# Optimization experiments

Measured on AMD Instinct MI355X. Metric: run time of the kernel, lower is better.

Reference implementation:

```python
import jax, jax.numpy as jnp
import numpy as np

N_NODES = 100000
N_EDGES = 1600000
DIM = 64
N_GRAPHS = 1000


def setup_inputs() -> dict:
    key = jax.random.key(0)
    ks = jax.random.split(key, 6)
    s = 1.0 / np.sqrt(DIM)
    x = jax.random.normal(ks[0], (N_NODES, DIM), dtype=jnp.float32)
    edge_index = jax.random.randint(ks[1], (2, N_EDGES), 0, N_NODES, dtype=jnp.int64)
    batch = jnp.sort(jax.random.randint(ks[2], (N_NODES,), 0, N_GRAPHS, dtype=jnp.int64))
    W1 = jax.random.normal(ks[3], (DIM, DIM), dtype=jnp.float32) * s
    b1 = jnp.zeros((DIM,), jnp.float32)
    W2 = jax.random.normal(ks[4], (DIM, DIM), dtype=jnp.float32) * s
    b2 = jnp.zeros((DIM,), jnp.float32)
    return {"x": x, "W1": W1, "b1": b1, "W2": W2, "b2": b2,
            "edge_index": edge_index, "batch": batch}


def reference(x, W1, b1, W2, b2, edge_index, batch):
    n = x.shape[0]
    loop = jnp.arange(n, dtype=edge_index.dtype)
    src = jnp.concatenate([edge_index[0], loop])  # [E+N] with self-loops
    dst = jnp.concatenate([edge_index[1], loop])
    # symmetric GCN normalization: deg^{-1/2}[src] * deg^{-1/2}[dst]
    deg = jax.ops.segment_sum(jnp.ones(src.shape[0], x.dtype), dst, num_segments=n)
    dinv = jax.lax.rsqrt(jnp.maximum(deg, 1.0))  # deg >= 1 due to self-loops
    norm = (dinv[src] * dinv[dst])[:, None]      # [E+N, 1]

    def gcn(h, W, b):
        h = h @ W                                  # transform first (smaller dim path)
        msg = h[src] * norm                        # gather + normalize
        return jax.ops.segment_sum(msg, dst, num_segments=n) + b

    h = jax.nn.relu(gcn(x, W1, b1))
    # dropout: eval mode -> identity
    h = jax.nn.relu(gcn(h, W2, b2))

    counts = jax.ops.segment_sum(jnp.ones((n,), x.dtype), batch, num_segments=N_GRAPHS)
    pooled = jax.ops.segment_sum(h, batch, num_segments=N_GRAPHS)
    return pooled / jnp.maximum(counts, 1.0)[:, None]
```

## Files before the change

kernel.cpp:

```cpp
#include <hip/hip_runtime.h>
#include <hip/hip_fp16.h>

#define DIM 64
#define BIN_SHIFT 7
#define BINSZ 128
#define MAXBINS 1024
#define PB 128

typedef __attribute__((ext_vector_type(2))) float floatx2;
typedef __attribute__((ext_vector_type(4))) float f32x4;
typedef __attribute__((ext_vector_type(8))) _Float16 f16x8;
typedef __attribute__((ext_vector_type(4))) _Float16 f16x4;


__global__ __launch_bounds__(256) void k_zero(int* __restrict__ bintot,
                                              float* __restrict__ out,
                                              int NB, int GD) {
    int i = blockIdx.x * 256 + threadIdx.x;
    if (i < NB) bintot[i] = 0;
    for (int j = i; j < GD; j += gridDim.x * 256) out[j] = 0.f;
}


__global__ __launch_bounds__(256) void k_hist2(const int* __restrict__ dst,
                                               int* __restrict__ bintot, int E, int NB) {
    __shared__ int h[MAXBINS];
    for (int i = threadIdx.x; i < NB; i += 256) h[i] = 0;
    __syncthreads();
    int per = (E + PB - 1) / PB;
    int e0 = blockIdx.x * per;
    int e1 = e0 + per; if (e1 > E) e1 = E;
    for (int e = e0 + (int)threadIdx.x; e < e1; e += 256)
        atomicAdd(&h[dst[e] >> BIN_SHIFT], 1);
    __syncthreads();
    for (int i = threadIdx.x; i < NB; i += 256)
        if (h[i]) atomicAdd(&bintot[i], h[i]);
}


__global__ __launch_bounds__(256) void k_scan782(const int* __restrict__ bintot,
                                                 int* __restrict__ binoff,
                                                 int* __restrict__ bincur, int NB, int E) {
    __shared__ int ws[4];
    int tid = threadIdx.x;
    int j0 = tid * 4;
    int v[4]; int sum = 0;
#pragma unroll
    for (int t = 0; t < 4; ++t) {
        int j = j0 + t;
        int x = (j < NB) ? bintot[j] : 0;
        v[t] = sum; sum += x;
    }
    int lane = tid & 63, wv = tid >> 6;
    int x = sum;
#pragma unroll
    for (int d = 1; d < 64; d <<= 1) {
        int t = __shfl_up(x, d);
        if (lane >= d) x += t;
    }
    if (lane == 63) ws[wv] = x;
    __syncthreads();
    int prefix = 0;
    for (int w = 0; w < wv; ++w) prefix += ws[w];
    int ex = prefix + x - sum;
#pragma unroll
    for (int t = 0; t < 4; ++t) {
        int j = j0 + t;
        if (j < NB) { binoff[j] = ex + v[t]; bincur[j] = ex + v[t]; }
    }
    if (tid == 255) binoff[NB] = prefix + x;
}


__global__ __launch_bounds__(256) void k_bucket2(const int* __restrict__ src,
                                                 const int* __restrict__ dst,
                                                 int* __restrict__ bincur,
                                                 int* __restrict__ bkt, int E, int NB) {
    __shared__ int cnt_[MAXBINS], base_[MAXBINS];
    int tid = threadIdx.x;
    for (int i = tid; i < NB; i += 256) cnt_[i] = 0;
    __syncthreads();
    int per = (E + PB - 1) / PB;
    int e0 = blockIdx.x * per;
    int e1 = e0 + per; if (e1 > E) e1 = E;
    for (int e = e0 + tid; e < e1; e += 256)
        atomicAdd(&cnt_[dst[e] >> BIN_SHIFT], 1);
    __syncthreads();
    for (int i = tid; i < NB; i += 256) {
        int c = cnt_[i];
        base_[i] = c ? atomicAdd(&bincur[i], c) : 0;
        cnt_[i] = 0;
    }
    __syncthreads();
    for (int e = e0 + tid; e < e1; e += 256) {
        int d = dst[e];
        int b = d >> BIN_SHIFT;
        int pos = base_[b] + atomicAdd(&cnt_[b], 1);
        bkt[pos] = src[e] | ((d & (BINSZ - 1)) << 24);
    }
}


__global__ __launch_bounds__(256) void k_binsort(const int* __restrict__ bkt,
                                                 const int* __restrict__ binoff,
                                                 int* __restrict__ csr,
                                                 int* __restrict__ off,
                                                 float* __restrict__ dinv,
                                                 const int* __restrict__ batch,
                                                 int* __restrict__ goff,
                                                 int N, int G, int E, int NB) {
    __shared__ int cnt[BINSZ], bas[BINSZ], cur[BINSZ];
    __shared__ int wsum[4];
    int tid = threadIdx.x;
    int b = blockIdx.x;
    int s0 = binoff[b];
    int s1 = binoff[b + 1];
    if (tid < BINSZ) { cnt[tid] = 0; cur[tid] = 0; }
    __syncthreads();
    for (int i = s0 + tid; i < s1; i += 256)
        atomicAdd(&cnt[(bkt[i] >> 24) & (BINSZ - 1)], 1);
    __syncthreads();
    int my = (tid < BINSZ) ? cnt[tid] : 0;
    int lane = tid & 63, wv = tid >> 6;
    int x = my;
#pragma unroll
    for (int d = 1; d < 64; d <<= 1) {
        int t = __shfl_up(x, d);
        if (lane >= d) x += t;
    }
    if (lane == 63) wsum[wv] = x;
    __syncthreads();
    int prefix = 0;
    for (int w = 0; w < wv; ++w) prefix += wsum[w];
    int ex = x + prefix - my;
    if (tid < BINSZ) {
        bas[tid] = ex;
        int v = (b << BIN_SHIFT) + tid;
        if (v < N) {
            off[v] = s0 + ex;
            dinv[v] = rsqrtf((float)(my + 1));
            if (v == N - 1) off[N] = E;
            int bb = batch[v];
            int prev = (v == 0) ? -1 : batch[v - 1];
            for (int g = prev + 1; g <= bb; ++g) goff[g] = v;
            if (v == N - 1)
                for (int g = bb + 1; g <= G; ++g) goff[g] = N;
        }
    }
    __syncthreads();
    for (int i = s0 + tid; i < s1; i += 256) {
        int p = bkt[i];
        int lo = (p >> 24) & (BINSZ - 1);
        int li = atomicAdd(&cur[lo], 1);
        csr[s0 + bas[lo] + li] = p & 0xFFFFFF;
    }
}


__global__ __launch_bounds__(256) void k_gemm(const float* __restrict__ X,
                                              const float* __restrict__ W,
                                              const float* __restrict__ dinv,
                                              unsigned int* __restrict__ Y8, int N) {
    __shared__ float Os[16 * 68];
    int tid = threadIdx.x;
    int lane = tid & 63, w = tid >> 6;
    int m = lane & 15, g = lane >> 4;
    int row0 = blockIdx.x * 16;
    int row = row0 + m;

    f16x8 B0, B1;
    {
        int n = (w << 4) + m;
        const float* wp = W + (g << 3) * 64 + n;
#pragma unroll
        for (int j = 0; j < 8; ++j) B0[j] = (_Float16)wp[j * 64];
        wp += 32 * 64;
#pragma unroll
        for (int j = 0; j < 8; ++j) B1[j] = (_Float16)wp[j * 64];
    }
    f16x8 A0, A1;
    {
        float4 u0 = make_float4(0.f, 0.f, 0.f, 0.f), u1 = u0, u2 = u0, u3 = u0;
        if (row < N) {
            const float* xp = X + (size_t)row * DIM + (g << 3);
            u0 = *(const float4*)(xp);
            u1 = *(const float4*)(xp + 4);
            u2 = *(const float4*)(xp + 32);
            u3 = *(const float4*)(xp + 36);
        }
        A0[0] = (_Float16)u0.x; A0[1] = (_Float16)u0.y; A0[2] = (_Float16)u0.z; A0[3] = (_Float16)u0.w;
        A0[4] = (_Float16)u1.x; A0[5] = (_Float16)u1.y; A0[6] = (_Float16)u1.z; A0[7] = (_Float16)u1.w;
        A1[0] = (_Float16)u2.x; A1[1] = (_Float16)u2.y; A1[2] = (_Float16)u2.z; A1[3] = (_Float16)u2.w;
        A1[4] = (_Float16)u3.x; A1[5] = (_Float16)u3.y; A1[6] = (_Float16)u3.z; A1[7] = (_Float16)u3.w;
    }
    f32x4 acc = {0.f, 0.f, 0.f, 0.f};
    acc = __builtin_amdgcn_mfma_f32_16x16x32_f16(A0, B0, acc, 0, 0, 0);
    acc = __builtin_amdgcn_mfma_f32_16x16x32_f16(A1, B1, acc, 0, 0, 0);
#pragma unroll
    for (int j = 0; j < 4; ++j)
        Os[((g << 2) + j) * 68 + (w << 4) + m] = acc[j];
    __syncthreads();

    int r = tid >> 4, c = tid & 15;
    int orow = row0 + r;
    if (orow < N) {
        float4 o = *(const float4*)(Os + r * 68 + (c << 2));
        float s = dinv[orow];
        int p = 0;
        p = __builtin_amdgcn_cvt_pk_fp8_f32(o.x * s, o.y * s, p, false);
        p = __builtin_amdgcn_cvt_pk_fp8_f32(o.z * s, o.w * s, p, true);
        Y8[(size_t)orow * 16 + c] = (unsigned int)p;
    } else if (orow == N) {
        Y8[(size_t)orow * 16 + c] = 0u;
    }
}


__device__ __forceinline__ float4 gather_rows(const unsigned int* __restrict__ hs8,
                                              const int* __restrict__ csr,
                                              int k0, int k1, int v, int l, int gw4,
                                              int N) {
    float4 a0, a1, a2, a3;
    {
        unsigned int u = hs8[(unsigned)((v << 4) | l)];
        floatx2 f0 = __builtin_amdgcn_cvt_pk_f32_fp8((int)u, false);
        floatx2 f1 = __builtin_amdgcn_cvt_pk_f32_fp8((int)u, true);
        a0 = make_float4(f0.x, f0.y, f1.x, f1.y);
        a1 = make_float4(0.f, 0.f, 0.f, 0.f);
        a2 = make_float4(0.f, 0.f, 0.f, 0.f);
        a3 = make_float4(0.f, 0.f, 0.f, 0.f);
    }
    for (int kb = k0; kb < k1; kb += 16) {
        int rem = k1 - kb;
        int idx = (l < rem) ? csr[kb + l] : N;
        unsigned uu[16];
#pragma unroll
        for (int t = 0; t < 16; ++t) {
            int s = __shfl(idx, gw4 + t);
            uu[t] = hs8[(unsigned)((s << 4) | l)];
        }
#pragma unroll
        for (int t = 0; t < 16; t += 4) {
            floatx2 q0 = __builtin_amdgcn_cvt_pk_f32_fp8((int)uu[t + 0], false);
            floatx2 q1 = __builtin_amdgcn_cvt_pk_f32_fp8((int)uu[t + 0], true);
            floatx2 q2 = __builtin_amdgcn_cvt_pk_f32_fp8((int)uu[t + 1], false);
            floatx2 q3 = __builtin_amdgcn_cvt_pk_f32_fp8((int)uu[t + 1], true);
            floatx2 q4 = __builtin_amdgcn_cvt_pk_f32_fp8((int)uu[t + 2], false);
            floatx2 q5 = __builtin_amdgcn_cvt_pk_f32_fp8((int)uu[t + 2], true);
            floatx2 q6 = __builtin_amdgcn_cvt_pk_f32_fp8((int)uu[t + 3], false);
            floatx2 q7 = __builtin_amdgcn_cvt_pk_f32_fp8((int)uu[t + 3], true);
            a0.x += q0.x; a0.y += q0.y; a0.z += q1.x; a0.w += q1.y;
            a1.x += q2.x; a1.y += q2.y; a1.z += q3.x; a1.w += q3.y;
            a2.x += q4.x; a2.y += q4.y; a2.z += q5.x; a2.w += q5.y;
            a3.x += q6.x; a3.y += q6.y; a3.z += q7.x; a3.w += q7.y;
        }
    }
    return make_float4(a0.x + a1.x + a2.x + a3.x,
                       a0.y + a1.y + a2.y + a3.y,
                       a0.z + a1.z + a2.z + a3.z,
                       a0.w + a1.w + a2.w + a3.w);
}


__global__ __launch_bounds__(256) void k_gather_gemm(const unsigned int* __restrict__ hs8,
                                                     const int* __restrict__ csr,
                                                     const int* __restrict__ off,
                                                     const float* __restrict__ dinv,
                                                     const float* __restrict__ bias,
                                                     const float* __restrict__ W,
                                                     unsigned int* __restrict__ hs_out,
                                                     int N) {
    __shared__ _Float16 Xs[16 * 72];
    __shared__ float Os[16 * 68];
    int tid = threadIdx.x;
    int r = tid >> 4, l = tid & 15;
    int lane = tid & 63, w = tid >> 6;
    int m = lane & 15, g = lane >> 4;
    int gw4 = (r & 3) << 4;
    int v = blockIdx.x * 16 + r;

    f16x8 B0, B1;
    {
        int n = (w << 4) + m;
        const float* wp = W + (g << 3) * 64 + n;
#pragma unroll
        for (int j = 0; j < 8; ++j) B0[j] = (_Float16)wp[j * 64];
        wp += 32 * 64;
#pragma unroll
        for (int j = 0; j < 8; ++j) B1[j] = (_Float16)wp[j * 64];
    }
    if (blockIdx.x == 0 && tid < 16)
        hs_out[(size_t)N * 16 + tid] = 0u;

    float dv = 0.f;
    float4 h = make_float4(0.f, 0.f, 0.f, 0.f);
    if (v < N) {
        dv = dinv[v];
        float4 bv = ((const float4*)bias)[l];
        float4 acc = gather_rows(hs8, csr, off[v], off[v + 1], v, l, gw4, N);
        h.x = fmaxf(acc.x * dv + bv.x, 0.f);
        h.y = fmaxf(acc.y * dv + bv.y, 0.f);
        h.z = fmaxf(acc.z * dv + bv.z, 0.f);
        h.w = fmaxf(acc.w * dv + bv.w, 0.f);
    }
    {
        f16x4 hv;
        hv[0] = (_Float16)h.x; hv[1] = (_Float16)h.y;
        hv[2] = (_Float16)h.z; hv[3] = (_Float16)h.w;
        *(f16x4*)(Xs + r * 72 + (l << 2)) = hv;
    }
    __syncthreads();

    f16x8 A0 = *(const f16x8*)(Xs + m * 72 + (g << 3));
    f16x8 A1 = *(const f16x8*)(Xs + m * 72 + 32 + (g << 3));
    f32x4 acc2 = {0.f, 0.f, 0.f, 0.f};
    acc2 = __builtin_amdgcn_mfma_f32_16x16x32_f16(A0, B0, acc2, 0, 0, 0);
    acc2 = __builtin_amdgcn_mfma_f32_16x16x32_f16(A1, B1, acc2, 0, 0, 0);
#pragma unroll
    for (int j = 0; j < 4; ++j)
        Os[((g << 2) + j) * 68 + (w << 4) + m] = acc2[j];
    __syncthreads();

    if (v < N) {
        float4 o = *(const float4*)(Os + r * 68 + (l << 2));
        int p = 0;
        p = __builtin_amdgcn_cvt_pk_fp8_f32(o.x * dv, o.y * dv, p, false);
        p = __builtin_amdgcn_cvt_pk_fp8_f32(o.z * dv, o.w * dv, p, true);
        hs_out[(size_t)v * 16 + l] = (unsigned int)p;
    }
}


__global__ __launch_bounds__(256) void k_gather_pool(const unsigned int* __restrict__ hs8,
                                                     const int* __restrict__ csr,
                                                     const int* __restrict__ off,
                                                     const float* __restrict__ dinv,
                                                     const float* __restrict__ bias,
                                                     const int* __restrict__ batch,
                                                     const int* __restrict__ goff,
                                                     float* __restrict__ out, int N) {
    __shared__ float vals[16][68];
    __shared__ int gid[16];
    int tid = threadIdx.x;
    int r = tid >> 4, l = tid & 15;
    int gw4 = (r & 3) << 4;
    int v = blockIdx.x * 16 + r;

    float4 val = make_float4(0.f, 0.f, 0.f, 0.f);
    int g = -1;
    if (v < N) {
        g = batch[v];
        float dv = dinv[v];
        float4 bv = ((const float4*)bias)[l];
        float4 acc = gather_rows(hs8, csr, off[v], off[v + 1], v, l, gw4, N);
        float inv = 1.0f / (float)(goff[g + 1] - goff[g]);
        val.x = fmaxf(acc.x * dv + bv.x, 0.f) * inv;
        val.y = fmaxf(acc.y * dv + bv.y, 0.f) * inv;
        val.z = fmaxf(acc.z * dv + bv.z, 0.f) * inv;
        val.w = fmaxf(acc.w * dv + bv.w, 0.f) * inv;
    }
    *(float4*)(&vals[r][l << 2]) = val;
    if (l == 0) gid[r] = g;
    __syncthreads();

    if (v < N) {
        bool leader = (r == 0) || (gid[r - 1] != g);
        if (leader) {
            float4 sacc = val;
            for (int rr = r + 1; rr < 16 && gid[rr] == g; ++rr) {
                float4 t = *(const float4*)(&vals[rr][l << 2]);
                sacc.x += t.x; sacc.y += t.y; sacc.z += t.z; sacc.w += t.w;
            }
            float* op = out + (size_t)g * DIM + (l << 2);
            atomicAdd(op + 0, sacc.x);
            atomicAdd(op + 1, sacc.y);
            atomicAdd(op + 2, sacc.z);
            atomicAdd(op + 3, sacc.w);
        }
    }
}


static inline int cdiv(int a, int b) { return (a + b - 1) / b; }

extern "C" void kernel_launch(void* const* d_in, const int* in_sizes, int n_in,
                              void* d_out, int out_size, void* d_ws, size_t ws_size,
                              hipStream_t stream) {
    const float* x   = (const float*)d_in[0];
    const float* W1  = (const float*)d_in[1];
    const float* b1  = (const float*)d_in[2];
    const float* W2  = (const float*)d_in[3];
    const float* b2  = (const float*)d_in[4];
    const int*   ei  = (const int*)d_in[5];
    const int*   bat = (const int*)d_in[6];

    const int N = in_sizes[0] / DIM;
    const int E = in_sizes[5] / 2;
    const int G = out_size / DIM;
    const int NB = cdiv(N, BINSZ);
    const int* src = ei;
    const int* dst = ei + E;
    float* out = (float*)d_out;

    __half* hs1    = (__half*)d_ws;
    __half* hs2    = hs1 + (size_t)(N + 1) * DIM;
    float*  dinv   = (float*)(hs2 + (size_t)(N + 1) * DIM);
    int*    off    = (int*)(dinv + N);
    int*    goff   = off + (N + 1);
    int*    bintot = goff + (G + 1);
    int*    binoff = bintot + MAXBINS;
    int*    bincur = binoff + (MAXBINS + 1);
    int*    csr    = bincur + MAXBINS;
    int*    bkt    = (int*)hs1;

    k_zero<<<256, 256, 0, stream>>>(bintot, out, NB, G * DIM);
    k_hist2<<<PB, 256, 0, stream>>>(dst, bintot, E, NB);
    k_scan782<<<1, 256, 0, stream>>>(bintot, binoff, bincur, NB, E);
    k_bucket2<<<PB, 256, 0, stream>>>(src, dst, bincur, bkt, E, NB);
    k_binsort<<<NB, 256, 0, stream>>>(bkt, binoff, csr, off, dinv, bat, goff, N, G, E, NB);

    k_gemm<<<cdiv(N + 1, 16), 256, 0, stream>>>(x, W1, dinv, (unsigned int*)hs1, N);

    k_gather_gemm<<<cdiv(N, 16), 256, 0, stream>>>((const unsigned int*)hs1, csr, off,
                                                   dinv, b1, W2, (unsigned int*)hs2, N);

    k_gather_pool<<<cdiv(N, 16), 256, 0, stream>>>((const unsigned int*)hs2, csr, off,
                                                   dinv, b2, bat, goff, out, N);
}
```

Baseline: 221.7 us.

## Replace two-level binned CSR build with global atomic counting sort

Replaces the histogram, bucket and per-bin LDS sort pipeline with a simpler counting sort. A per-node degree pass uses global atomics, a two-kernel block scan builds offsets (also computing dinv and graph offsets), and a scatter places each source into CSR through a global atomicAdd on the per-node cursor. This drops the intermediate bucket array and the bin-sort kernel. In exchange it trades LDS atomics and localized writes for millions of global atomics and random scattered CSR writes, and neighbour order within a row becomes nondeterministic.

New measurement: 349.3 us. +57.6%, slower.

```diff
diff --git a/kernel.cpp b/kernel.cpp
--- a/kernel.cpp
+++ b/kernel.cpp
@@ -2,10 +2,6 @@
 #include <hip/hip_fp16.h>
 
 #define DIM 64
-#define BIN_SHIFT 7
-#define BINSZ 128
-#define MAXBINS 1024
-#define PB 128
 
 typedef __attribute__((ext_vector_type(2))) float floatx2;
 typedef __attribute__((ext_vector_type(4))) float f32x4;
@@ -13,42 +9,36 @@
 typedef __attribute__((ext_vector_type(4))) _Float16 f16x4;
 
 
-__global__ __launch_bounds__(256) void k_zero(int* __restrict__ bintot,
+__global__ __launch_bounds__(256) void k_zero(int* __restrict__ deg,
                                               float* __restrict__ out,
-                                              int NB, int GD) {
+                                              int N, int GD) {
     int i = blockIdx.x * 256 + threadIdx.x;
-    if (i < NB) bintot[i] = 0;
-    for (int j = i; j < GD; j += gridDim.x * 256) out[j] = 0.f;
-}
-
-
-__global__ __launch_bounds__(256) void k_hist2(const int* __restrict__ dst,
-                                               int* __restrict__ bintot, int E, int NB) {
-    __shared__ int h[MAXBINS];
-    for (int i = threadIdx.x; i < NB; i += 256) h[i] = 0;
-    __syncthreads();
-    int per = (E + PB - 1) / PB;
-    int e0 = blockIdx.x * per;
-    int e1 = e0 + per; if (e1 > E) e1 = E;
-    for (int e = e0 + (int)threadIdx.x; e < e1; e += 256)
-        atomicAdd(&h[dst[e] >> BIN_SHIFT], 1);
-    __syncthreads();
-    for (int i = threadIdx.x; i < NB; i += 256)
-        if (h[i]) atomicAdd(&bintot[i], h[i]);
-}
-
-
-__global__ __launch_bounds__(256) void k_scan782(const int* __restrict__ bintot,
-                                                 int* __restrict__ binoff,
-                                                 int* __restrict__ bincur, int NB, int E) {
-    __shared__ int ws[4];
+    int stride = gridDim.x * 256;
+    for (int j = i; j < N; j += stride) deg[j] = 0;
+    for (int j = i; j < GD; j += stride) out[j] = 0.f;
+}
+
+
+__global__ __launch_bounds__(256) void k_deg(const int* __restrict__ dst,
+                                             int* __restrict__ deg, int E) {
+    int i = blockIdx.x * 256 + threadIdx.x;
+    int stride = gridDim.x * 256;
+    for (int e = i; e < E; e += stride)
+        atomicAdd(&deg[dst[e]], 1);
+}
+
+
+__global__ __launch_bounds__(1024) void k_scanA2(const int* __restrict__ deg,
+                                                 int* __restrict__ off,
+                                                 int* __restrict__ bsums, int N) {
+    __shared__ int ws[16];
     int tid = threadIdx.x;
-    int j0 = tid * 4;
+    int j0 = blockIdx.x * 4096 + tid * 4;
     int v[4]; int sum = 0;
 #pragma unroll
     for (int t = 0; t < 4; ++t) {
         int j = j0 + t;
-        int x = (j < NB) ? bintot[j] : 0;
+        int x = (j < N) ? deg[j] : 0;
         v[t] = sum; sum += x;
     }
     int lane = tid & 63, wv = tid >> 6;
@@ -66,93 +56,53 @@
 #pragma unroll
     for (int t = 0; t < 4; ++t) {
         int j = j0 + t;
-        if (j < NB) { binoff[j] = ex + v[t]; bincur[j] = ex + v[t]; }
-    }
-    if (tid == 255) binoff[NB] = prefix + x;
-}
-
-
-__global__ __launch_bounds__(256) void k_bucket2(const int* __restrict__ src,
+        if (j < N) off[j] = ex + v[t];
+    }
+    if (tid == 1023) bsums[blockIdx.x] = prefix + x;
+}
+
+
+__global__ __launch_bounds__(1024) void k_scanC(int* __restrict__ off,
+                                                int* __restrict__ cur,
+                                                const int* __restrict__ bsums,
+                                                const int* __restrict__ deg,
+                                                const int* __restrict__ batch,
+                                                float* __restrict__ dinv,
+                                                int* __restrict__ goff,
+                                                int N, int G, int E) {
+    int blk = blockIdx.x;
+    int base = 0;
+    for (int w = 0; w < blk; ++w) base += bsums[w];
+    int j = blk * 4096 + threadIdx.x;
+#pragma unroll
+    for (int t = 0; t < 4; ++t, j += 1024) {
+        if (j < N) {
+            int o = off[j] + base;
+            off[j] = o;
+            cur[j] = o;
+            dinv[j] = rsqrtf((float)(deg[j] + 1));
+            int bb = batch[j];
+            int prev = (j == 0) ? -1 : batch[j - 1];
+            for (int g = prev + 1; g <= bb; ++g) goff[g] = j;
+            if (j == N - 1) {
+                off[N] = E;
+                for (int g = bb + 1; g <= G; ++g) goff[g] = N;
+            }
+        }
+    }
+}
+
+
+__global__ __launch_bounds__(256) void k_scatter(const int* __restrict__ src,
                                                  const int* __restrict__ dst,
-                                                 int* __restrict__ bincur,
-                                                 int* __restrict__ bkt, int E, int NB) {
-    __shared__ int cnt_[MAXBINS], base_[MAXBINS];
-    int tid = threadIdx.x;
-    for (int i = tid; i < NB; i += 256) cnt_[i] = 0;
-    __syncthreads();
-    int per = (E + PB - 1) / PB;
-    int e0 = blockIdx.x * per;
-    int e1 = e0 + per; if (e1 > E) e1 = E;
-    for (int e = e0 + tid; e < e1; e += 256)
-        atomicAdd(&cnt_[dst[e] >> BIN_SHIFT], 1);
-    __syncthreads();
-    for (int i = tid; i < NB; i += 256) {
-        int c = cnt_[i];
-        base_[i] = c ? atomicAdd(&bincur[i], c) : 0;
-        cnt_[i] = 0;
-    }
-    __syncthreads();
-    for (int e = e0 + tid; e < e1; e += 256) {
+                                                 int* __restrict__ cur,
+                                                 int* __restrict__ csr, int E) {
+    int i = blockIdx.x * 256 + threadIdx.x;
+    int stride = gridDim.x * 256;
+    for (int e = i; e < E; e += stride) {
         int d = dst[e];
-        int b = d >> BIN_SHIFT;
-        int pos = base_[b] + atomicAdd(&cnt_[b], 1);
-        bkt[pos] = src[e] | ((d & (BINSZ - 1)) << 24);
-    }
-}
-
-
-__global__ __launch_bounds__(256) void k_binsort(const int* __restrict__ bkt,
-                                                 const int* __restrict__ binoff,
-                                                 int* __restrict__ csr,
-                                                 int* __restrict__ off,
-                                                 float* __restrict__ dinv,
-                                                 const int* __restrict__ batch,
-                                                 int* __restrict__ goff,
-                                                 int N, int G, int E, int NB) {
-    __shared__ int cnt[BINSZ], bas[BINSZ], cur[BINSZ];
-    __shared__ int wsum[4];
-    int tid = threadIdx.x;
-    int b = blockIdx.x;
-    int s0 = binoff[b];
-    int s1 = binoff[b + 1];
-    if (tid < BINSZ) { cnt[tid] = 0; cur[tid] = 0; }
-    __syncthreads();
-    for (int i = s0 + tid; i < s1; i += 256)
-        atomicAdd(&cnt[(bkt[i] >> 24) & (BINSZ - 1)], 1);
-    __syncthreads();
-    int my = (tid < BINSZ) ? cnt[tid] : 0;
-    int lane = tid & 63, wv = tid >> 6;
-    int x = my;
-#pragma unroll
-    for (int d = 1; d < 64; d <<= 1) {
-        int t = __shfl_up(x, d);
-        if (lane >= d) x += t;
-    }
-    if (lane == 63) wsum[wv] = x;
-    __syncthreads();
-    int prefix = 0;
-    for (int w = 0; w < wv; ++w) prefix += wsum[w];
-    int ex = x + prefix - my;
-    if (tid < BINSZ) {
-        bas[tid] = ex;
-        int v = (b << BIN_SHIFT) + tid;
-        if (v < N) {
-            off[v] = s0 + ex;
-            dinv[v] = rsqrtf((float)(my + 1));
-            if (v == N - 1) off[N] = E;
-            int bb = batch[v];
-            int prev = (v == 0) ? -1 : batch[v - 1];
-            for (int g = prev + 1; g <= bb; ++g) goff[g] = v;
-            if (v == N - 1)
-                for (int g = bb + 1; g <= G; ++g) goff[g] = N;
-        }
-    }
-    __syncthreads();
-    for (int i = s0 + tid; i < s1; i += 256) {
-        int p = bkt[i];
-        int lo = (p >> 24) & (BINSZ - 1);
-        int li = atomicAdd(&cur[lo], 1);
-        csr[s0 + bas[lo] + li] = p & 0xFFFFFF;
+        int pos = atomicAdd(&cur[d], 1);
+        csr[pos] = src[e];
     }
 }
 
@@ -397,7 +347,6 @@
     const int N = in_sizes[0] / DIM;
     const int E = in_sizes[5] / 2;
     const int G = out_size / DIM;
-    const int NB = cdiv(N, BINSZ);
     const int* src = ei;
     const int* dst = ei + E;
     float* out = (float*)d_out;
@@ -406,18 +355,18 @@
     __half* hs2    = hs1 + (size_t)(N + 1) * DIM;
     float*  dinv   = (float*)(hs2 + (size_t)(N + 1) * DIM);
     int*    off    = (int*)(dinv + N);
-    int*    goff   = off + (N + 1);
-    int*    bintot = goff + (G + 1);
-    int*    binoff = bintot + MAXBINS;
-    int*    bincur = binoff + (MAXBINS + 1);
-    int*    csr    = bincur + MAXBINS;
-    int*    bkt    = (int*)hs1;
-
-    k_zero<<<256, 256, 0, stream>>>(bintot, out, NB, G * DIM);
-    k_hist2<<<PB, 256, 0, stream>>>(dst, bintot, E, NB);
-    k_scan782<<<1, 256, 0, stream>>>(bintot, binoff, bincur, NB, E);
-    k_bucket2<<<PB, 256, 0, stream>>>(src, dst, bincur, bkt, E, NB);
-    k_binsort<<<NB, 256, 0, stream>>>(bkt, binoff, csr, off, dinv, bat, goff, N, G, E, NB);
+    int*    cur    = off + (N + 1);
+    int*    goff   = cur + N;
+    int*    deg    = goff + (G + 1);
+    int*    bsums  = deg + N;
+    int*    csr    = bsums + 64;
+
+    k_zero<<<512, 256, 0, stream>>>(deg, out, N, G * DIM);
+    k_deg<<<2048, 256, 0, stream>>>(dst, deg, E);
+    int nblk = cdiv(N, 4096);
+    k_scanA2<<<nblk, 1024, 0, stream>>>(deg, off, bsums, N);
+    k_scanC<<<nblk, 1024, 0, stream>>>(off, cur, bsums, deg, bat, dinv, goff, N, G, E);
+    k_scatter<<<2048, 256, 0, stream>>>(src, dst, cur, csr, E);
 
     k_gemm<<<cdiv(N + 1, 16), 256, 0, stream>>>(x, W1, dinv, (unsigned int*)hs1, N);
 
```
